# Kernel tuning notes

Hardware: AMD Instinct MI355X
Metric: run time of the kernel (lower is better)

Reference implementation:

```python
import jax, jax.numpy as jnp
import numpy as np

D = 1024
H = 16
DK = D // H


def apply_rope(x):
    # x: [B, H, T, dk]; interleaved-pair RoPE as in the torch source
    T, dim = x.shape[-2], x.shape[-1]
    inv_freq = 1.0 / (10000.0 ** (jnp.arange(0, dim, 2, dtype=x.dtype) / dim))  # [dk/2]
    pos = jnp.arange(T, dtype=x.dtype)
    sinusoid = pos[:, None] * inv_freq[None, :]  # [T, dk/2]
    sin, cos = jnp.sin(sinusoid), jnp.cos(sinusoid)
    x1, x2 = x[..., ::2], x[..., 1::2]
    rot = jnp.stack([x1 * cos - x2 * sin, x1 * sin + x2 * cos], axis=-1)
    return rot.reshape(x.shape)


def setup_inputs() -> dict:
    key = jax.random.key(0)
    k1, k2, k3, k4, k5 = jax.random.split(key, 5)
    B, T = 2, 2048
    s = 1.0 / np.sqrt(D)
    return {
        "x": jax.random.normal(k1, (B, T, D), dtype=jnp.float32),
        "W_qkv": jax.random.normal(k2, (D, 3 * D), dtype=jnp.float32) * s,
        "b_qkv": jnp.zeros((3 * D,), dtype=jnp.float32),
        "W_out": jax.random.normal(k3, (D, D), dtype=jnp.float32) * s,
        "b_out": jnp.zeros((D,), dtype=jnp.float32),
    }


def reference(x, W_qkv, b_qkv, W_out, b_out):
    B, T, C = x.shape
    qkv = x @ W_qkv + b_qkv  # [B, T, 3D]
    qkv = qkv.reshape(B, T, 3, H, DK).transpose(2, 0, 3, 1, 4)  # [3, B, H, T, dk]
    q, k, v = qkv[0], qkv[1], qkv[2]
    q, k = apply_rope(q), apply_rope(k)
    scores = jnp.einsum("bhtd,bhsd->bhts", q, k) / jnp.sqrt(jnp.asarray(DK, x.dtype))
    causal = jnp.tril(jnp.ones((T, T), dtype=bool))
    scores = jnp.where(causal, scores, jnp.asarray(-1e9, x.dtype))
    probs = jax.nn.softmax(scores, axis=-1)
    attn = jnp.einsum("bhts,bhsd->bhtd", probs, v)  # [B, H, T, dk]
    out = attn.transpose(0, 2, 1, 3).reshape(B, T, C)  # b h t d -> b t (h d)
    return out @ W_out + b_out
```

## Files before the change

### kernel.cpp

```cpp
#include <hip/hip_runtime.h>
#include <math.h>

#define DMODEL 1024
#define NHEAD  16
#define HDK    64
#define BATCH  2
#define SEQ    2048
#define MROWS  (BATCH*SEQ)
#define NQKV   (3*DMODEL)
#define LOG2_10000 13.287712379549449f
#define INV2PI 0.15915494309189535f
#define SCALE_LOG2E 0.1803368801111137f
#define M_FIX 8.0f

typedef __attribute__((ext_vector_type(8))) short bf16x8;
typedef __attribute__((ext_vector_type(4))) float f32x4;

__device__ __forceinline__ short f2bf(float f) {
    union { float f; unsigned u; } v; v.f = f;
    unsigned r = v.u + 0x7fffu + ((v.u >> 16) & 1u);
    return (short)(r >> 16);
}

__device__ __forceinline__ float fast_exp2(float x) {
#if __has_builtin(__builtin_amdgcn_exp2f)
    return __builtin_amdgcn_exp2f(x);
#else
    return exp2f(x);
#endif
}

__device__ __forceinline__ void gld_lds16(const short* g, short* l) {
    __builtin_amdgcn_global_load_lds(
        (const __attribute__((address_space(1))) void*)g,
        (__attribute__((address_space(3))) void*)l, 16, 0, 0);
}

__global__ __launch_bounds__(256) void prep_kernel(
    const float* __restrict__ x, const float* __restrict__ wqkv,
    const float* __restrict__ wout,
    short* __restrict__ xb, short* __restrict__ wqkv_t, short* __restrict__ wout_t)
{
    __shared__ short tile[32][33];
    const int tid = threadIdx.x;
    if (blockIdx.x < 2048) {
        const int i = (blockIdx.x * 256 + tid) * 8;
        float4 a = *(const float4*)(x + i);
        float4 b = *(const float4*)(x + i + 4);
        bf16x8 o;
        o[0] = f2bf(a.x); o[1] = f2bf(a.y); o[2] = f2bf(a.z); o[3] = f2bf(a.w);
        o[4] = f2bf(b.x); o[5] = f2bf(b.y); o[6] = f2bf(b.z); o[7] = f2bf(b.w);
        *(bf16x8*)(xb + i) = o;
        return;
    }
    const int bx = blockIdx.x - 2048;
    int nx = bx & 127;
    const int ky = bx >> 7;
    const float* in; short* out; int N;
    if (nx < 96) { in = wqkv; out = wqkv_t; N = NQKV; }
    else         { in = wout; out = wout_t; N = DMODEL; nx -= 96; }
    const int tx = tid & 31, ty = tid >> 5;
    const int n0 = nx * 32, k0 = ky * 32;
    #pragma unroll
    for (int i = 0; i < 32; i += 8)
        tile[ty + i][tx] = f2bf(in[(size_t)(k0 + ty + i) * N + n0 + tx]);
    __syncthreads();
    #pragma unroll
    for (int i = 0; i < 32; i += 8)
        out[(size_t)(n0 + ty + i) * DMODEL + k0 + tx] = tile[tx][ty + i];
}

__global__ __launch_bounds__(256) void qkv_gemm_kernel(
    const short* __restrict__ xb, const short* __restrict__ Wt,
    const float* __restrict__ bias,
    short* __restrict__ qd, short* __restrict__ kd, short* __restrict__ vtb)
{
    __shared__ __align__(16) short As[128 * 32];
    __shared__ __align__(16) short Bs[128 * 32];
    const int tid = threadIdx.x;
    const int lane = tid & 63, wave = tid >> 6;
    const int wm = wave & 1, wn = wave >> 1;
    const int l15 = lane & 15, quad = lane >> 4;
    const int n0 = blockIdx.x * 128, m0 = blockIdx.y * 128;
    const int srow = lane >> 2, sc = lane & 3;

    const short* gA1 = xb + (size_t)(m0 + wave * 32 + srow) * DMODEL + sc * 8;
    const short* gA2 = gA1 + (size_t)16 * DMODEL;
    const short* gB1 = Wt + (size_t)(n0 + wave * 32 + srow) * DMODEL + sc * 8;
    const short* gB2 = gB1 + (size_t)16 * DMODEL;
    short* lA1 = As + (wave * 32) * 32;
    short* lA2 = As + (wave * 32 + 16) * 32;
    short* lB1 = Bs + (wave * 32) * 32;
    short* lB2 = Bs + (wave * 32 + 16) * 32;

    f32x4 zero = {0.f, 0.f, 0.f, 0.f};
    f32x4 acc[4][4];
    #pragma unroll
    for (int i = 0; i < 4; ++i)
        #pragma unroll
        for (int j = 0; j < 4; ++j) acc[i][j] = zero;

    for (int k0 = 0; k0 < DMODEL; k0 += 32) {
        __syncthreads();
        gld_lds16(gA1 + k0, lA1);
        gld_lds16(gA2 + k0, lA2);
        gld_lds16(gB1 + k0, lB1);
        gld_lds16(gB2 + k0, lB2);
        __syncthreads();
        bf16x8 af[4], bfr[4];
        #pragma unroll
        for (int i = 0; i < 4; ++i)
            af[i] = *(const bf16x8*)&As[(wm * 64 + i * 16 + l15) * 32 + quad * 8];
        #pragma unroll
        for (int j = 0; j < 4; ++j)
            bfr[j] = *(const bf16x8*)&Bs[(wn * 64 + j * 16 + l15) * 32 + quad * 8];
        #pragma unroll
        for (int i = 0; i < 4; ++i)
            #pragma unroll
            for (int j = 0; j < 4; ++j)
                acc[i][j] = __builtin_amdgcn_mfma_f32_16x16x32_bf16(af[i], bfr[j], acc[i][j], 0, 0, 0);
    }

    const int which = n0 >> 10;
    float biasv[4], invf[4];
    int hh[4], dd[4];
    #pragma unroll
    for (int j = 0; j < 4; ++j) {
        const int n = n0 + wn * 64 + j * 16 + l15;
        biasv[j] = bias[n];
        hh[j] = (n & 1023) >> 6;
        dd[j] = n & 63;
        invf[j] = INV2PI * exp2f(-((float)(dd[j] & ~1) / 64.f) * LOG2_10000);
    }
    #pragma unroll
    for (int i = 0; i < 4; ++i) {
        #pragma unroll
        for (int r = 0; r < 4; ++r) {
            const int m = m0 + wm * 64 + i * 16 + quad * 4 + r;
            const int b = m >> 11, t = m & (SEQ - 1);
            #pragma unroll
            for (int j = 0; j < 4; ++j) {
                float val = acc[i][j][r] + biasv[j];
                if (which < 2) {
                    const float rev = (float)t * invf[j];
                    const float fr = rev - floorf(rev);
                    const float s = __builtin_amdgcn_sinf(fr);
                    const float c = __builtin_amdgcn_cosf(fr);
                    const float partner = __shfl_xor(val, 1);
                    val = (lane & 1) ? (partner * s + val * c) : (val * c - partner * s);
                    short* dst = (which == 0) ? qd : kd;
                    dst[((size_t)(b * NHEAD + hh[j]) * SEQ + t) * HDK + dd[j]] = f2bf(val);
                } else {
                    vtb[((size_t)(b * NHEAD + hh[j]) * HDK + dd[j]) * SEQ + t] = f2bf(val);
                }
            }
        }
    }
}

__global__ __launch_bounds__(256) void attn_mfma_kernel(
    const short* __restrict__ qd, const short* __restrict__ kd,
    const short* __restrict__ vt, short* __restrict__ od)
{
    __shared__ __align__(16) short Ks[2][2][64 * 32];
    __shared__ __align__(16) short Vs[2][2][64 * 32];
    __shared__ __align__(16) short Ps[4][16][72];
    const int tid = threadIdx.x, lane = tid & 63, w = tid >> 6;
    const int l15 = lane & 15, quad = lane >> 4;
    const int id = (int)blockIdx.x;
    const int c = id & 7, kk = id >> 3;
    const int qp = kk & 15, jj = kk >> 4;
    const int hb = c + 8 * jj;
    const int h = hb & 15, b = hb >> 4;
    const size_t base = ((size_t)(b * NHEAD + h)) * SEQ * HDK;
    const int srow = tid >> 2, sc = tid & 3;
    const int lofs = tid * 8;
    f32x4 zero = {0.f, 0.f, 0.f, 0.f};

    const int qtile[2] = { qp, 31 - qp };
    const short* kp0 = kd + base + (size_t)srow * HDK + sc * 8;
    const short* vp0 = vt + base + (size_t)srow * SEQ + sc * 8;
    const short* kp1 = kp0 + (size_t)64 * HDK;
    const short* vp1 = vp0 + 64;

    #pragma unroll 1
    for (int qi = 0; qi < 2; ++qi) {
        const int q0 = qtile[qi] * 64;
        bf16x8 qf[2];
        {
            const short* qrow = qd + base + (size_t)(q0 + w * 16 + l15) * HDK;
            qf[0] = *(const bf16x8*)(qrow + quad * 8);
            qf[1] = *(const bf16x8*)(qrow + 32 + quad * 8);
        }
        float l_acc[4] = {0.f, 0.f, 0.f, 0.f};
        f32x4 o[4];
        #pragma unroll
        for (int j = 0; j < 4; ++j) o[j] = zero;

        const int nkt = q0 / 64 + 1;
        const int npair = (nkt + 1) >> 1;

        bf16x8 rk[2][2], rv[2][2];
        rk[0][0] = *(const bf16x8*)kp0; rk[0][1] = *(const bf16x8*)(kp0 + 32);
        rv[0][0] = *(const bf16x8*)vp0; rv[0][1] = *(const bf16x8*)(vp0 + 32);
        rk[1][0] = *(const bf16x8*)kp1; rk[1][1] = *(const bf16x8*)(kp1 + 32);
        rv[1][0] = *(const bf16x8*)vp1; rv[1][1] = *(const bf16x8*)(vp1 + 32);

        for (int p = 0; p < npair; ++p) {
            __syncthreads();
            *(bf16x8*)&Ks[0][0][lofs] = rk[0][0]; *(bf16x8*)&Ks[0][1][lofs] = rk[0][1];
            *(bf16x8*)&Vs[0][0][lofs] = rv[0][0]; *(bf16x8*)&Vs[0][1][lofs] = rv[0][1];
            *(bf16x8*)&Ks[1][0][lofs] = rk[1][0]; *(bf16x8*)&Ks[1][1][lofs] = rk[1][1];
            *(bf16x8*)&Vs[1][0][lofs] = rv[1][0]; *(bf16x8*)&Vs[1][1][lofs] = rv[1][1];
            __syncthreads();
            if (p + 1 < npair) {
                const int sn = (2 * p + 2) * 64;
                const short* kn = kd + base + (size_t)(sn + srow) * HDK + sc * 8;
                const short* vn = vt + base + (size_t)srow * SEQ + sn + sc * 8;
                rk[0][0] = *(const bf16x8*)kn; rk[0][1] = *(const bf16x8*)(kn + 32);
                rv[0][0] = *(const bf16x8*)vn; rv[0][1] = *(const bf16x8*)(vn + 32);
                const short* kn2 = kn + (size_t)64 * HDK;
                const short* vn2 = vn + 64;
                rk[1][0] = *(const bf16x8*)kn2; rk[1][1] = *(const bf16x8*)(kn2 + 32);
                rv[1][0] = *(const bf16x8*)vn2; rv[1][1] = *(const bf16x8*)(vn2 + 32);
            } else if (qi == 0) {
                rk[0][0] = *(const bf16x8*)kp0; rk[0][1] = *(const bf16x8*)(kp0 + 32);
                rv[0][0] = *(const bf16x8*)vp0; rv[0][1] = *(const bf16x8*)(vp0 + 32);
                rk[1][0] = *(const bf16x8*)kp1; rk[1][1] = *(const bf16x8*)(kp1 + 32);
                rv[1][0] = *(const bf16x8*)vp1; rv[1][1] = *(const bf16x8*)(vp1 + 32);
            }

            #pragma unroll
            for (int tt = 0; tt < 2; ++tt) {
                const int kt = 2 * p + tt;
                if (tt == 1 && kt >= nkt) break;
                f32x4 sacc[4];
                #pragma unroll
                for (int j = 0; j < 4; ++j) {
                    bf16x8 kf0 = *(const bf16x8*)&Ks[tt][0][(j * 16 + l15) * 32 + quad * 8];
                    bf16x8 kf1 = *(const bf16x8*)&Ks[tt][1][(j * 16 + l15) * 32 + quad * 8];
                    sacc[j] = __builtin_amdgcn_mfma_f32_16x16x32_bf16(qf[0], kf0, zero, 0, 0, 0);
                    sacc[j] = __builtin_amdgcn_mfma_f32_16x16x32_bf16(qf[1], kf1, sacc[j], 0, 0, 0);
                }
                if (kt == nkt - 1) {
                    const int s0 = kt * 64;
                    #pragma unroll
                    for (int j = 0; j < 4; ++j) {
                        const int scol = s0 + j * 16 + l15;
                        #pragma unroll
                        for (int r = 0; r < 4; ++r) {
                            const int trow = q0 + w * 16 + quad * 4 + r;
                            const float sv = sacc[j][r] * SCALE_LOG2E - M_FIX;
                            const float pv = (scol > trow) ? 0.f : fast_exp2(sv);
                            l_acc[r] += pv;
                            Ps[w][quad * 4 + r][j * 16 + l15] = f2bf(pv);
                        }
                    }
                } else {
                    #pragma unroll
                    for (int j = 0; j < 4; ++j)
                        #pragma unroll
                        for (int r = 0; r < 4; ++r) {
                            const float pv = fast_exp2(sacc[j][r] * SCALE_LOG2E - M_FIX);
                            l_acc[r] += pv;
                            Ps[w][quad * 4 + r][j * 16 + l15] = f2bf(pv);
                        }
                }
                bf16x8 pf0 = *(const bf16x8*)&Ps[w][l15][quad * 8];
                bf16x8 pf1 = *(const bf16x8*)&Ps[w][l15][32 + quad * 8];
                #pragma unroll
                for (int j = 0; j < 4; ++j) {
                    bf16x8 vf0 = *(const bf16x8*)&Vs[tt][0][(j * 16 + l15) * 32 + quad * 8];
                    bf16x8 vf1 = *(const bf16x8*)&Vs[tt][1][(j * 16 + l15) * 32 + quad * 8];
                    o[j] = __builtin_amdgcn_mfma_f32_16x16x32_bf16(pf0, vf0, o[j], 0, 0, 0);
                    o[j] = __builtin_amdgcn_mfma_f32_16x16x32_bf16(pf1, vf1, o[j], 0, 0, 0);
                }
            }
        }

        #pragma unroll
        for (int r = 0; r < 4; ++r) {
            float sr = l_acc[r];
            #pragma unroll
            for (int off = 1; off < 16; off <<= 1) sr += __shfl_xor(sr, off);
            l_acc[r] = sr;
        }
        #pragma unroll
        for (int r = 0; r < 4; ++r) {
            const float inv = 1.f / l_acc[r];
            const int t = q0 + w * 16 + quad * 4 + r;
            #pragma unroll
            for (int j = 0; j < 4; ++j)
                od[((size_t)(b * SEQ + t) * NHEAD + h) * HDK + j * 16 + l15] =
                    f2bf(o[j][r] * inv);
        }
    }
}

__global__ __launch_bounds__(256) void out_gemm_kernel(
    const short* __restrict__ Ab, const short* __restrict__ Wt,
    const float* __restrict__ bias, float* __restrict__ out)
{
    __shared__ __align__(16) short As[128 * 32];
    __shared__ __align__(16) short Bs[128 * 32];
    const int tid = threadIdx.x;
    const int lane = tid & 63, wave = tid >> 6;
    const int wm = wave & 1, wn = wave >> 1;
    const int l15 = lane & 15, quad = lane >> 4;
    const int n0 = blockIdx.x * 128, m0 = blockIdx.y * 128;
    const int srow = lane >> 2, sc = lane & 3;

    const short* gA1 = Ab + (size_t)(m0 + wave * 32 + srow) * DMODEL + sc * 8;
    const short* gA2 = gA1 + (size_t)16 * DMODEL;
    const short* gB1 = Wt + (size_t)(n0 + wave * 32 + srow) * DMODEL + sc * 8;
    const short* gB2 = gB1 + (size_t)16 * DMODEL;
    short* lA1 = As + (wave * 32) * 32;
    short* lA2 = As + (wave * 32 + 16) * 32;
    short* lB1 = Bs + (wave * 32) * 32;
    short* lB2 = Bs + (wave * 32 + 16) * 32;

    f32x4 zero = {0.f, 0.f, 0.f, 0.f};
    f32x4 acc[4][4];
    #pragma unroll
    for (int i = 0; i < 4; ++i)
        #pragma unroll
        for (int j = 0; j < 4; ++j) acc[i][j] = zero;

    for (int k0 = 0; k0 < DMODEL; k0 += 32) {
        __syncthreads();
        gld_lds16(gA1 + k0, lA1);
        gld_lds16(gA2 + k0, lA2);
        gld_lds16(gB1 + k0, lB1);
        gld_lds16(gB2 + k0, lB2);
        __syncthreads();
        bf16x8 af[4], bfr[4];
        #pragma unroll
        for (int i = 0; i < 4; ++i)
            af[i] = *(const bf16x8*)&As[(wm * 64 + i * 16 + l15) * 32 + quad * 8];
        #pragma unroll
        for (int j = 0; j < 4; ++j)
            bfr[j] = *(const bf16x8*)&Bs[(wn * 64 + j * 16 + l15) * 32 + quad * 8];
        #pragma unroll
        for (int i = 0; i < 4; ++i)
            #pragma unroll
            for (int j = 0; j < 4; ++j)
                acc[i][j] = __builtin_amdgcn_mfma_f32_16x16x32_bf16(af[i], bfr[j], acc[i][j], 0, 0, 0);
    }

    #pragma unroll
    for (int j = 0; j < 4; ++j) {
        const int n = n0 + wn * 64 + j * 16 + l15;
        const float bv = bias[n];
        #pragma unroll
        for (int i = 0; i < 4; ++i)
            #pragma unroll
            for (int r = 0; r < 4; ++r) {
                const int m = m0 + wm * 64 + i * 16 + quad * 4 + r;
                out[(size_t)m * DMODEL + n] = acc[i][j][r] + bv;
            }
    }
}

extern "C" void kernel_launch(void* const* d_in, const int* in_sizes, int n_in,
                              void* d_out, int out_size, void* d_ws, size_t ws_size,
                              hipStream_t stream) {
    const float* x    = (const float*)d_in[0];
    const float* Wqkv = (const float*)d_in[1];
    const float* bqkv = (const float*)d_in[2];
    const float* Wout = (const float*)d_in[3];
    const float* bout = (const float*)d_in[4];
    float* out = (float*)d_out;

    short* ws = (short*)d_ws;
    short* xb     = ws;
    short* wqkv_t = xb + (size_t)4 * 1024 * 1024;
    short* wout_t = wqkv_t + (size_t)3 * 1024 * 1024;
    short* qd     = wout_t + (size_t)1024 * 1024;
    short* kd     = qd + (size_t)4 * 1024 * 1024;
    short* vtb    = kd + (size_t)4 * 1024 * 1024;
    short* attn   = vtb + (size_t)4 * 1024 * 1024;

    prep_kernel<<<2048 + 4096, 256, 0, stream>>>(x, Wqkv, Wout, xb, wqkv_t, wout_t);

    qkv_gemm_kernel<<<dim3(NQKV / 128, MROWS / 128), 256, 0, stream>>>(
        xb, wqkv_t, bqkv, qd, kd, vtb);

    attn_mfma_kernel<<<512, 256, 0, stream>>>(qd, kd, vtb, attn);

    out_gemm_kernel<<<dim3(DMODEL / 128, MROWS / 128), 256, 0, stream>>>(
        attn, wout_t, bout, out);
}
```

Baseline: 196.0 us.

## Batch QK MFMAs for both key tiles and pack P stores via cvt_pk_bf16

```diff
diff --git a/kernel.cpp b/kernel.cpp
--- a/kernel.cpp
+++ b/kernel.cpp
@@ -20,6 +20,12 @@
     union { float f; unsigned u; } v; v.f = f;
     unsigned r = v.u + 0x7fffu + ((v.u >> 16) & 1u);
     return (short)(r >> 16);
+}
+
+__device__ __forceinline__ unsigned pk_bf16(float a, float b) {
+    unsigned d;
+    asm("v_cvt_pk_bf16_f32 %0, %1, %2" : "=v"(d) : "v"(a), "v"(b));
+    return d;
 }
 
 __device__ __forceinline__ float fast_exp2(float x) {
@@ -164,7 +170,7 @@
 {
     __shared__ __align__(16) short Ks[2][2][64 * 32];
     __shared__ __align__(16) short Vs[2][2][64 * 32];
-    __shared__ __align__(16) short Ps[4][16][72];
+    __shared__ __align__(16) short Ps[4][2][16][72];
     const int tid = threadIdx.x, lane = tid & 63, w = tid >> 6;
     const int l15 = lane & 15, quad = lane >> 4;
     const int id = (int)blockIdx.x;
@@ -175,6 +181,7 @@
     const size_t base = ((size_t)(b * NHEAD + h)) * SEQ * HDK;
     const int srow = tid >> 2, sc = tid & 3;
     const int lofs = tid * 8;
+    const int odd = l15 & 1;
     f32x4 zero = {0.f, 0.f, 0.f, 0.f};
 
     const int qtile[2] = { qp, 31 - qp };
@@ -207,6 +214,7 @@
         rv[1][0] = *(const bf16x8*)vp1; rv[1][1] = *(const bf16x8*)(vp1 + 32);
 
         for (int p = 0; p < npair; ++p) {
+            const bool has2 = (2 * p + 1 < nkt);
             __syncthreads();
             *(bf16x8*)&Ks[0][0][lofs] = rk[0][0]; *(bf16x8*)&Ks[0][1][lofs] = rk[0][1];
             *(bf16x8*)&Vs[0][0][lofs] = rv[0][0]; *(bf16x8*)&Vs[0][1][lofs] = rv[0][1];
@@ -230,18 +238,28 @@
                 rv[1][0] = *(const bf16x8*)vp1; rv[1][1] = *(const bf16x8*)(vp1 + 32);
             }
 
-            #pragma unroll
-            for (int tt = 0; tt < 2; ++tt) {
-                const int kt = 2 * p + tt;
-                if (tt == 1 && kt >= nkt) break;
-                f32x4 sacc[4];
+            f32x4 sacc[2][4];
+            #pragma unroll
+            for (int j = 0; j < 4; ++j) {
+                bf16x8 kf0 = *(const bf16x8*)&Ks[0][0][(j * 16 + l15) * 32 + quad * 8];
+                bf16x8 kf1 = *(const bf16x8*)&Ks[0][1][(j * 16 + l15) * 32 + quad * 8];
+                sacc[0][j] = __builtin_amdgcn_mfma_f32_16x16x32_bf16(qf[0], kf0, zero, 0, 0, 0);
+                sacc[0][j] = __builtin_amdgcn_mfma_f32_16x16x32_bf16(qf[1], kf1, sacc[0][j], 0, 0, 0);
+            }
+            if (has2) {
                 #pragma unroll
                 for (int j = 0; j < 4; ++j) {
-                    bf16x8 kf0 = *(const bf16x8*)&Ks[tt][0][(j * 16 + l15) * 32 + quad * 8];
-                    bf16x8 kf1 = *(const bf16x8*)&Ks[tt][1][(j * 16 + l15) * 32 + quad * 8];
-                    sacc[j] = __builtin_amdgcn_mfma_f32_16x16x32_bf16(qf[0], kf0, zero, 0, 0, 0);
-                    sacc[j] = __builtin_amdgcn_mfma_f32_16x16x32_bf16(qf[1], kf1, sacc[j], 0, 0, 0);
+                    bf16x8 kf0 = *(const bf16x8*)&Ks[1][0][(j * 16 + l15) * 32 + quad * 8];
+                    bf16x8 kf1 = *(const bf16x8*)&Ks[1][1][(j * 16 + l15) * 32 + quad * 8];
+                    sacc[1][j] = __builtin_amdgcn_mfma_f32_16x16x32_bf16(qf[0], kf0, zero, 0, 0, 0);
+                    sacc[1][j] = __builtin_amdgcn_mfma_f32_16x16x32_bf16(qf[1], kf1, sacc[1][j], 0, 0, 0);
                 }
+            }
+
+            const int ntt = has2 ? 2 : 1;
+            for (int tt = 0; tt < ntt; ++tt) {
+                const int kt = 2 * p + tt;
+                float pr[4][4];
                 if (kt == nkt - 1) {
                     const int s0 = kt * 64;
                     #pragma unroll
@@ -250,10 +268,10 @@
                         #pragma unroll
                         for (int r = 0; r < 4; ++r) {
                             const int trow = q0 + w * 16 + quad * 4 + r;
-                            const float sv = sacc[j][r] * SCALE_LOG2E - M_FIX;
+                            const float sv = sacc[tt][j][r] * SCALE_LOG2E - M_FIX;
                             const float pv = (scol > trow) ? 0.f : fast_exp2(sv);
+                            pr[j][r] = pv;
                             l_acc[r] += pv;
-                            Ps[w][quad * 4 + r][j * 16 + l15] = f2bf(pv);
                         }
                     }
                 } else {
@@ -261,13 +279,34 @@
                     for (int j = 0; j < 4; ++j)
                         #pragma unroll
                         for (int r = 0; r < 4; ++r) {
-                            const float pv = fast_exp2(sacc[j][r] * SCALE_LOG2E - M_FIX);
+                            const float pv = fast_exp2(sacc[tt][j][r] * SCALE_LOG2E - M_FIX);
+                            pr[j][r] = pv;
                             l_acc[r] += pv;
-                            Ps[w][quad * 4 + r][j * 16 + l15] = f2bf(pv);
                         }
                 }
-                bf16x8 pf0 = *(const bf16x8*)&Ps[w][l15][quad * 8];
-                bf16x8 pf1 = *(const bf16x8*)&Ps[w][l15][32 + quad * 8];
+                #pragma unroll
+                for (int j = 0; j < 4; ++j) {
+                    const float q0v = __shfl_xor(pr[j][0], 1);
+                    const float q1v = __shfl_xor(pr[j][1], 1);
+                    const float q2v = __shfl_xor(pr[j][2], 1);
+                    const float q3v = __shfl_xor(pr[j][3], 1);
+                    const float a0 = odd ? q2v : pr[j][0];
+                    const float b0 = odd ? pr[j][2] : q0v;
+                    const float a1 = odd ? q3v : pr[j][1];
+                    const float b1 = odd ? pr[j][3] : q1v;
+                    const unsigned d0 = pk_bf16(a0, b0);
+                    const unsigned d1 = pk_bf16(a1, b1);
+                    const int row = quad * 4 + odd * 2;
+                    const int col = j * 16 + (l15 & ~1);
+                    *(unsigned*)&Ps[w][tt][row][col] = d0;
+                    *(unsigned*)&Ps[w][tt][row + 1][col] = d1;
+                }
+            }
+
+            #pragma unroll 1
+            for (int tt = 0; tt < ntt; ++tt) {
+                bf16x8 pf0 = *(const bf16x8*)&Ps[w][tt][l15][quad * 8];
+                bf16x8 pf1 = *(const bf16x8*)&Ps[w][tt][l15][32 + quad * 8];
                 #pragma unroll
                 for (int j = 0; j < 4; ++j) {
                     bf16x8 vf0 = *(const bf16x8*)&Vs[tt][0][(j * 16 + l15) * 32 + quad * 8];
```

Measured after the change: 205.0 us. 4.6% more time.
